# Optimization experiments

Hardware: AMD Instinct MI355X
Metric: run time of the kernel (lower is better)

The kernel has to match this reference:

```python
import jax, jax.numpy as jnp
import numpy as np

FEATURE_SIZES = [300, 1000, 1000, 500, 150, 12, 31, 30, 200, 50000, 50000, 20000, 100000]
# sections per table index i (from feature_sizes_dict -> feature_sections_dict in original)
SECTIONS = [(0, 1), (1, 2), (2, 3), (3, 4), (4, 5), (5, 6), (6, 7), (7, 10),
            (10, 24), (26, 28), (28, 30), (24, 26), (30, 45)]
N, F, E = 8192, 45, 256
_perm, _tbl = [], []
for _i, (_a, _b) in enumerate(SECTIONS):
    for _j in range(_a, _b):
        _perm.append(_j)
        _tbl.append(_i)
PERM = np.array(_perm)              # original Xi column for field position p (concat order)
TBL = np.array(_tbl)                # table index for field position p
OFFSETS = np.concatenate([[0], np.cumsum(FEATURE_SIZES)[:-1]]).astype(np.int32)
FIELD_OFF = OFFSETS[TBL]            # row offset into concatenated table per field position
TOTAL_V = int(np.sum(FEATURE_SIZES))  # 223273
VOCAB_COL = np.zeros(F, np.int32)
VOCAB_COL[PERM] = np.array(FEATURE_SIZES, np.int32)[TBL]  # per-column valid vocab for Xi


def setup_inputs() -> dict:
    key = jax.random.key(0)
    ks = jax.random.split(key, 10)
    Xi = jax.random.randint(ks[0], (N, F), 0, jnp.asarray(VOCAB_COL), dtype=jnp.int32)
    Xv = jax.random.uniform(ks[1], (N, F), dtype=jnp.float32)
    W1 = jax.random.normal(ks[2], (TOTAL_V, 1), dtype=jnp.float32) * 0.01
    W2 = jax.random.normal(ks[3], (TOTAL_V, E), dtype=jnp.float32) * 0.01
    bias = jax.random.normal(ks[4], (1,), dtype=jnp.float32)
    l1_w = jax.random.normal(ks[5], (32, F * E), dtype=jnp.float32) * 0.02
    l1_b = jnp.zeros((32,), jnp.float32)
    l2_w = jax.random.normal(ks[6], (32, 32), dtype=jnp.float32) * 0.02
    l2_b = jnp.zeros((32,), jnp.float32)
    return {"Xi": Xi, "Xv": Xv, "W1": W1, "W2": W2, "bias": bias,
            "l1_w": l1_w, "l1_b": l1_b, "bn1_g": jnp.ones((32,), jnp.float32),
            "bn1_b": jnp.zeros((32,), jnp.float32), "l2_w": l2_w, "l2_b": l2_b,
            "bn2_g": jnp.ones((32,), jnp.float32), "bn2_b": jnp.zeros((32,), jnp.float32)}


def _batchnorm(x, g, b, eps=1e-5):
    # training-mode BN: biased batch statistics (PyTorch normalization convention)
    m = x.mean(0)
    v = x.var(0)
    return (x - m) * jax.lax.rsqrt(v + eps) * g + b


def reference(Xi, Xv, W1, W2, bias, l1_w, l1_b, bn1_g, bn1_b, l2_w, l2_b, bn2_g, bn2_b):
    perm = jnp.asarray(PERM)
    foff = jnp.asarray(FIELD_OFF)
    idx = Xi[:, perm] + foff[None, :]          # (N, 45) rows into concatenated tables
    xv = Xv[:, perm]                            # (N, 45) values in concat order
    # first-order: scalar embedding * value per field
    fm_first = W1[idx, 0] * xv                  # (N, 45)
    # second-order: E-dim embedding * value per field
    e = W2[idx] * xv[:, :, None]                # (N, 45, E)
    s = e.sum(axis=1)                           # (N, E)
    fm_second = 0.5 * (s * s - (e * e).sum(axis=1))  # (N, E)
    # deep part (concat of per-field 2nd-order embs, in original loop order)
    deep = e.reshape(e.shape[0], -1)            # (N, 45*E)
    h = _batchnorm(deep @ l1_w.T + l1_b, bn1_g, bn1_b)
    h = _batchnorm(h @ l2_w.T + l2_b, bn2_g, bn2_b)  # (N, 32); no final num_classes linear in original
    return fm_first.sum(axis=1) + fm_second.sum(axis=1) + h.sum(axis=1) + bias  # (N,)
```

## Files before the change

### kernel.cpp

```cpp
#include <hip/hip_runtime.h>
#include <hip/hip_bf16.h>

#define NS 8192
#define NF 45
#define ED 256
#define L1K 11520
#define NH 32

typedef __attribute__((ext_vector_type(8))) short bf16x8;
typedef __attribute__((ext_vector_type(4))) float f32x4;
typedef __attribute__((ext_vector_type(4))) unsigned uint32x4;

__constant__ int c_perm[NF] = {
    0,1,2,3,4,5,6,7,8,9,
    10,11,12,13,14,15,16,17,18,19,20,21,22,23,
    26,27, 28,29, 24,25,
    30,31,32,33,34,35,36,37,38,39,40,41,42,43,44};
__constant__ int c_foff[NF] = {
    0,300,1300,2300,2800,2950,2962,2993,2993,2993,
    3023,3023,3023,3023,3023,3023,3023,3023,3023,3023,3023,3023,3023,3023,
    3223,3223, 53223,53223, 103223,103223,
    123223,123223,123223,123223,123223,123223,123223,123223,
    123223,123223,123223,123223,123223,123223,123223};

__device__ __forceinline__ short f2bf(float x) {
    unsigned u = __builtin_bit_cast(unsigned, x);
    u += 0x7fffu + ((u >> 16) & 1u);
    return (short)(u >> 16);
}

__device__ __forceinline__ unsigned pk_bf16(float a, float b) {
    unsigned r;
    asm("v_cvt_pk_bf16_f32 %0, %1, %2" : "=v"(r) : "v"(a), "v"(b));
    return r;
}

__global__ __launch_bounds__(256) void k_pack(const float* __restrict__ l1w,
                                              short* __restrict__ bfrag) {
    int t = blockIdx.x * 256 + threadIdx.x;
    if (t >= NF * 8192) return;
    int i  = t & 7;
    int l  = (t >> 3) & 63;
    int nt = (t >> 9) & 1;
    int ks = (t >> 10) & 7;
    int f  = t >> 13;
    int kout = nt * 16 + (l & 15);
    int col  = f * 256 + ks * 32 + (l >> 4) * 8 + i;
    bfrag[t] = f2bf(l1w[kout * L1K + col]);
}

__global__ __launch_bounds__(256, 4) void k_main(const float* __restrict__ W2,
                                                 const float* __restrict__ W1,
                                                 const int* __restrict__ Xi,
                                                 const float* __restrict__ Xv,
                                                 const short* __restrict__ bfrag,
                                                 float* __restrict__ h1h,
                                                 float* __restrict__ parth) {
    __shared__ int   s_idx[16 * NF];
    __shared__ float s_xv [16 * NF];
    __shared__ float s_red[4 * 16 * NH];
    __shared__ float s_q[4][16];
    __shared__ float s_fm1[16];

    const int tid  = threadIdx.x;
    const int w    = tid >> 6;
    const int l    = tid & 63;
    const int m    = l & 15;
    const int g4   = l >> 4;
    const int half = blockIdx.x & 1;
    const int n0   = (blockIdx.x >> 1) * 16;
    const int ks   = half * 4 + w;

    for (int t = tid; t < 16 * NF; t += 256) {
        int f = t % NF;
        int n = n0 + t / NF;
        int col = c_perm[f];
        s_idx[t] = Xi[n * NF + col] + c_foff[f];
        s_xv[t]  = Xv[n * NF + col];
    }
    __syncthreads();

    f32x4 acc0 = {0.f, 0.f, 0.f, 0.f};
    f32x4 acc1 = {0.f, 0.f, 0.f, 0.f};
    float sA[8];
    #pragma unroll
    for (int i = 0; i < 8; ++i) sA[i] = 0.f;
    float esq = 0.f, fm1 = 0.f;

    const short* bbase = bfrag + (size_t)ks * 1024 + l * 8;
    const float* wbase = W2 + ks * 32 + g4 * 8;
    const bool  isw0   = (half == 0 && w == 0);
    const int   mNF    = m * NF;

#define LOADF(ff, A0, A1, B0, B1, XV, W1R)                          \
    do {                                                            \
        int idx_ = s_idx[mNF + (ff)];                               \
        XV = s_xv[mNF + (ff)];                                      \
        const float* wr_ = wbase + (size_t)idx_ * ED;               \
        A0 = *(const f32x4*)(wr_);                                  \
        A1 = *(const f32x4*)(wr_ + 4);                              \
        const short* bp_ = bbase + (size_t)(ff) * 8192;             \
        B0 = *(const bf16x8*)(bp_);                                 \
        B1 = *(const bf16x8*)(bp_ + 512);                           \
        W1R = isw0 ? W1[idx_] : 0.f;                                \
    } while (0)

#define COMPF(A0, A1, B0, B1, XV, W1R)                              \
    do {                                                            \
        float e0 = A0.x * XV, e1 = A0.y * XV, e2 = A0.z * XV, e3 = A0.w * XV; \
        float e4 = A1.x * XV, e5 = A1.y * XV, e6 = A1.z * XV, e7 = A1.w * XV; \
        sA[0] += e0; sA[1] += e1; sA[2] += e2; sA[3] += e3;         \
        sA[4] += e4; sA[5] += e5; sA[6] += e6; sA[7] += e7;         \
        esq += e0 * e0; esq += e1 * e1; esq += e2 * e2; esq += e3 * e3; \
        esq += e4 * e4; esq += e5 * e5; esq += e6 * e6; esq += e7 * e7; \
        uint32x4 au_;                                               \
        au_.x = pk_bf16(e0, e1);                                    \
        au_.y = pk_bf16(e2, e3);                                    \
        au_.z = pk_bf16(e4, e5);                                    \
        au_.w = pk_bf16(e6, e7);                                    \
        bf16x8 Af_ = __builtin_bit_cast(bf16x8, au_);               \
        acc0 = __builtin_amdgcn_mfma_f32_16x16x32_bf16(Af_, B0, acc0, 0, 0, 0); \
        acc1 = __builtin_amdgcn_mfma_f32_16x16x32_bf16(Af_, B1, acc1, 0, 0, 0); \
        fm1 += W1R * XV;                                            \
    } while (0)

    f32x4  A0a, A1a, A0b, A1b, A0c, A1c;
    bf16x8 B0a, B1a, B0b, B1b, B0c, B1c;
    float  XVa, XVb, XVc, W1a, W1b, W1c;

    LOADF(0, A0a, A1a, B0a, B1a, XVa, W1a);
    LOADF(1, A0b, A1b, B0b, B1b, XVb, W1b);
    LOADF(2, A0c, A1c, B0c, B1c, XVc, W1c);

    for (int f = 0; f < NF - 3; f += 3) {
        COMPF(A0a, A1a, B0a, B1a, XVa, W1a);
        LOADF(f + 3, A0a, A1a, B0a, B1a, XVa, W1a);
        COMPF(A0b, A1b, B0b, B1b, XVb, W1b);
        LOADF(f + 4, A0b, A1b, B0b, B1b, XVb, W1b);
        COMPF(A0c, A1c, B0c, B1c, XVc, W1c);
        LOADF(f + 5, A0c, A1c, B0c, B1c, XVc, W1c);
    }
    COMPF(A0a, A1a, B0a, B1a, XVa, W1a);
    COMPF(A0b, A1b, B0b, B1b, XVb, W1b);
    COMPF(A0c, A1c, B0c, B1c, XVc, W1c);

#undef LOADF
#undef COMPF

    float q = -esq;
    #pragma unroll
    for (int i = 0; i < 8; ++i) q += sA[i] * sA[i];
    q += __shfl_xor(q, 16);
    q += __shfl_xor(q, 32);
    if (l < 16) s_q[w][l] = q;
    if (w == 0 && l < 16) s_fm1[l] = fm1;

    #pragma unroll
    for (int r = 0; r < 4; ++r) {
        s_red[w * 512 + (g4 * 4 + r) * 32 +      m] = acc0[r];
        s_red[w * 512 + (g4 * 4 + r) * 32 + 16 + m] = acc1[r];
    }
    __syncthreads();

    float* h1out = h1h + (size_t)half * NS * NH;
    for (int t = tid; t < 512; t += 256) {
        float v = s_red[t] + s_red[512 + t] + s_red[1024 + t] + s_red[1536 + t];
        h1out[(size_t)n0 * NH + t] = v;
    }
    if (tid < 16) {
        float fm2 = 0.5f * (s_q[0][tid] + s_q[1][tid] + s_q[2][tid] + s_q[3][tid]);
        parth[half * NS + n0 + tid] = s_fm1[tid] + fm2;
    }
}

__global__ __launch_bounds__(256) void k_stats(const float* __restrict__ h1h,
                                               float* __restrict__ S1,
                                               float* __restrict__ S2) {
    __shared__ float hc[64 * NH];
    const int tid = threadIdx.x;
    const int base = blockIdx.x * 64;
    for (int t = tid; t < 64 * NH; t += 256)
        hc[t] = h1h[(size_t)base * NH + t] + h1h[(size_t)NS * NH + base * NH + t];
    __syncthreads();

    const int j = tid >> 3;
    const int ks = (tid & 7) * 4;
    float a0 = 0.f, a1 = 0.f, a2 = 0.f, a3 = 0.f;
    for (int n = 0; n < 64; ++n) {
        float hj = hc[n * NH + j];
        f32x4 h = *(const f32x4*)&hc[n * NH + ks];
        a0 += hj * h.x; a1 += hj * h.y; a2 += hj * h.z; a3 += hj * h.w;
    }
    atomicAdd(&S2[j * NH + ks + 0], a0);
    atomicAdd(&S2[j * NH + ks + 1], a1);
    atomicAdd(&S2[j * NH + ks + 2], a2);
    atomicAdd(&S2[j * NH + ks + 3], a3);
    if (tid < NH) {
        float s = 0.f;
        for (int n = 0; n < 64; ++n) s += hc[n * NH + tid];
        atomicAdd(&S1[tid], s);
    }
}

__global__ __launch_bounds__(256) void k_coef(const float* __restrict__ S1,
                                              const float* __restrict__ S2,
                                              const float* __restrict__ g1,
                                              const float* __restrict__ l2w,
                                              const float* __restrict__ g2,
                                              const float* __restrict__ b2,
                                              const float* __restrict__ bias,
                                              float* __restrict__ cvec,
                                              float* __restrict__ k0out) {
    __shared__ float m1[NH], d1[NH], g2r2[NH], csh[NH];
    __shared__ float s2s[NH * NH];
    const int t = threadIdx.x;
    const float invN = 1.f / (float)NS;
    for (int i = t; i < NH * NH; i += 256) s2s[i] = S2[i];
    __syncthreads();
    if (t < NH) {
        float mm = S1[t] * invN;
        float v1 = s2s[t * NH + t] * invN - mm * mm;
        m1[t] = mm;
        d1[t] = g1[t] * rsqrtf(v1 + 1e-5f);
    }
    __syncthreads();
    if (t < NH) {
        float aw[NH];
        float p = 0.f;
        for (int j = 0; j < NH; ++j) { aw[j] = l2w[t * NH + j] * d1[j]; p += aw[j] * m1[j]; }
        float v2 = 0.f;
        for (int j = 0; j < NH; ++j) {
            float acc = 0.f;
            for (int j2 = 0; j2 < NH; ++j2) acc += aw[j2] * s2s[j * NH + j2];
            v2 += aw[j] * acc;
        }
        v2 = v2 * invN - p * p;
        g2r2[t] = g2[t] * rsqrtf(v2 + 1e-5f);
    }
    __syncthreads();
    if (t < NH) {
        float s = 0.f;
        for (int k = 0; k < NH; ++k) s += g2r2[k] * l2w[k * NH + t];
        float c = d1[t] * s;
        csh[t] = c;
        cvec[t] = c;
    }
    __syncthreads();
    if (t == 0) {
        float k0 = bias[0];
        for (int k = 0; k < NH; ++k) k0 += b2[k];
        for (int j = 0; j < NH; ++j) k0 -= csh[j] * m1[j];
        k0out[0] = k0;
    }
}

__global__ __launch_bounds__(256) void k_final(const float* __restrict__ h1h,
                                               const float* __restrict__ parth,
                                               const float* __restrict__ cvec,
                                               const float* __restrict__ k0p,
                                               float* __restrict__ out) {
    __shared__ float c[NH];
    __shared__ float k0s;
    const int t = threadIdx.x;
    if (t < NH) c[t] = cvec[t];
    if (t == 0) k0s = k0p[0];
    __syncthreads();
    const int n = blockIdx.x * 256 + t;
    const f32x4* hp0 = (const f32x4*)(h1h + (size_t)n * NH);
    const f32x4* hp1 = (const f32x4*)(h1h + (size_t)NS * NH + (size_t)n * NH);
    float dot = 0.f;
    #pragma unroll
    for (int q = 0; q < 8; ++q) {
        f32x4 h0 = hp0[q];
        f32x4 h1 = hp1[q];
        dot += (h0.x + h1.x) * c[q * 4]     + (h0.y + h1.y) * c[q * 4 + 1]
             + (h0.z + h1.z) * c[q * 4 + 2] + (h0.w + h1.w) * c[q * 4 + 3];
    }
    out[n] = parth[n] + parth[NS + n] + dot + k0s;
}

extern "C" void kernel_launch(void* const* d_in, const int* in_sizes, int n_in,
                              void* d_out, int out_size, void* d_ws, size_t ws_size,
                              hipStream_t stream) {
    const int*   Xi   = (const int*)  d_in[0];
    const float* Xv   = (const float*)d_in[1];
    const float* W1   = (const float*)d_in[2];
    const float* W2   = (const float*)d_in[3];
    const float* bias = (const float*)d_in[4];
    const float* l1w  = (const float*)d_in[5];
    const float* g1   = (const float*)d_in[7];
    const float* l2w  = (const float*)d_in[9];
    const float* g2   = (const float*)d_in[11];
    const float* b2   = (const float*)d_in[12];
    float* out = (float*)d_out;

    char* ws = (char*)d_ws;
    short* bfrag = (short*)ws;
    float* h1h   = (float*)(ws + (size_t)368640 * 2);
    float* parth = h1h + (size_t)2 * NS * NH;
    float* S1    = parth + 2 * NS;
    float* S2    = S1 + NH;
    float* cvec  = S2 + NH * NH;
    float* k0p   = cvec + NH;

    hipMemsetAsync(S1, 0, (NH + NH * NH) * sizeof(float), stream);
    k_pack <<<(NF * 8192 + 255) / 256, 256, 0, stream>>>(l1w, bfrag);
    k_main <<<NS / 16 * 2, 256, 0, stream>>>(W2, W1, Xi, Xv, bfrag, h1h, parth);
    k_stats<<<128, 256, 0, stream>>>(h1h, S1, S2);
    k_coef <<<1, 256, 0, stream>>>(S1, S2, g1, l2w, g2, b2, bias, cvec, k0p);
    k_final<<<NS / 256, 256, 0, stream>>>(h1h, parth, cvec, k0p, out);
}
```

Before: 380.7 us.

## Process 32 rows per 512-thread block covering full embedding dim, reuse B fragments

Each k_main block now handles 32 samples across all 8 k-slices of the embedding (8 waves) instead of 16 samples split over two half-blocks. Each wave loads a B fragment once and reuses it for two 16-row MFMA groups, halving l1 weight fragment traffic per sample. The result is a single h1h/parth buffer, so the stats and final kernels read half as much. In exchange, register pressure per thread roughly doubles, the grid shrinks to 256 blocks, and the shared reduction across 8 waves is larger.

```diff
diff --git a/kernel.cpp b/kernel.cpp
--- a/kernel.cpp
+++ b/kernel.cpp
@@ -49,29 +49,27 @@
     bfrag[t] = f2bf(l1w[kout * L1K + col]);
 }
 
-__global__ __launch_bounds__(256, 4) void k_main(const float* __restrict__ W2,
+__global__ __launch_bounds__(512, 2) void k_main(const float* __restrict__ W2,
                                                  const float* __restrict__ W1,
                                                  const int* __restrict__ Xi,
                                                  const float* __restrict__ Xv,
                                                  const short* __restrict__ bfrag,
                                                  float* __restrict__ h1h,
                                                  float* __restrict__ parth) {
-    __shared__ int   s_idx[16 * NF];
-    __shared__ float s_xv [16 * NF];
-    __shared__ float s_red[4 * 16 * NH];
-    __shared__ float s_q[4][16];
-    __shared__ float s_fm1[16];
-
-    const int tid  = threadIdx.x;
-    const int w    = tid >> 6;
-    const int l    = tid & 63;
-    const int m    = l & 15;
-    const int g4   = l >> 4;
-    const int half = blockIdx.x & 1;
-    const int n0   = (blockIdx.x >> 1) * 16;
-    const int ks   = half * 4 + w;
-
-    for (int t = tid; t < 16 * NF; t += 256) {
+    __shared__ int   s_idx[32 * NF];
+    __shared__ float s_xv [32 * NF];
+    __shared__ float s_red[8 * 32 * 33];
+    __shared__ float s_q[8 * 32];
+    __shared__ float s_fm1[32];
+
+    const int tid = threadIdx.x;
+    const int w   = tid >> 6;
+    const int l   = tid & 63;
+    const int m   = l & 15;
+    const int g4  = l >> 4;
+    const int n0  = blockIdx.x * 32;
+
+    for (int t = tid; t < 32 * NF; t += 512) {
         int f = t % NF;
         int n = n0 + t / NF;
         int col = c_perm[f];
@@ -80,96 +78,116 @@
     }
     __syncthreads();
 
-    f32x4 acc0 = {0.f, 0.f, 0.f, 0.f};
-    f32x4 acc1 = {0.f, 0.f, 0.f, 0.f};
-    float sA[8];
+    f32x4 acc00 = {0.f,0.f,0.f,0.f}, acc01 = {0.f,0.f,0.f,0.f};
+    f32x4 acc10 = {0.f,0.f,0.f,0.f}, acc11 = {0.f,0.f,0.f,0.f};
+    float sA0[8], sA1[8];
     #pragma unroll
-    for (int i = 0; i < 8; ++i) sA[i] = 0.f;
-    float esq = 0.f, fm1 = 0.f;
-
-    const short* bbase = bfrag + (size_t)ks * 1024 + l * 8;
-    const float* wbase = W2 + ks * 32 + g4 * 8;
-    const bool  isw0   = (half == 0 && w == 0);
+    for (int i = 0; i < 8; ++i) { sA0[i] = 0.f; sA1[i] = 0.f; }
+    float esq0 = 0.f, esq1 = 0.f, fm10 = 0.f, fm11 = 0.f;
+
+    const short* bbase = bfrag + (size_t)w * 1024 + l * 8;
+    const float* wbase = W2 + w * 32 + g4 * 8;
+    const bool  isw0   = (w == 0);
     const int   mNF    = m * NF;
-
-#define LOADF(ff, A0, A1, B0, B1, XV, W1R)                          \
+    const int   mNF1   = (m + 16) * NF;
+
+#define LOADF(ff, A00_,A01_,A10_,A11_,B0_,B1_,XV0_,XV1_,W10_,W11_)  \
     do {                                                            \
-        int idx_ = s_idx[mNF + (ff)];                               \
-        XV = s_xv[mNF + (ff)];                                      \
-        const float* wr_ = wbase + (size_t)idx_ * ED;               \
-        A0 = *(const f32x4*)(wr_);                                  \
-        A1 = *(const f32x4*)(wr_ + 4);                              \
+        int i0_ = s_idx[mNF  + (ff)];                               \
+        int i1_ = s_idx[mNF1 + (ff)];                               \
+        XV0_ = s_xv[mNF  + (ff)];                                   \
+        XV1_ = s_xv[mNF1 + (ff)];                                   \
+        const float* p0_ = wbase + (size_t)i0_ * ED;                \
+        const float* p1_ = wbase + (size_t)i1_ * ED;                \
+        A00_ = *(const f32x4*)(p0_);  A01_ = *(const f32x4*)(p0_ + 4); \
+        A10_ = *(const f32x4*)(p1_);  A11_ = *(const f32x4*)(p1_ + 4); \
         const short* bp_ = bbase + (size_t)(ff) * 8192;             \
-        B0 = *(const bf16x8*)(bp_);                                 \
-        B1 = *(const bf16x8*)(bp_ + 512);                           \
-        W1R = isw0 ? W1[idx_] : 0.f;                                \
+        B0_ = *(const bf16x8*)(bp_);                                \
+        B1_ = *(const bf16x8*)(bp_ + 512);                          \
+        W10_ = isw0 ? W1[i0_] : 0.f;                                \
+        W11_ = isw0 ? W1[i1_] : 0.f;                                \
     } while (0)
 
-#define COMPF(A0, A1, B0, B1, XV, W1R)                              \
+#define COMPG(A0_,A1_,B0_,B1_,XV_,SA_,ESQ_,ACC0_,ACC1_,FM_,W1R_)    \
     do {                                                            \
-        float e0 = A0.x * XV, e1 = A0.y * XV, e2 = A0.z * XV, e3 = A0.w * XV; \
-        float e4 = A1.x * XV, e5 = A1.y * XV, e6 = A1.z * XV, e7 = A1.w * XV; \
-        sA[0] += e0; sA[1] += e1; sA[2] += e2; sA[3] += e3;         \
-        sA[4] += e4; sA[5] += e5; sA[6] += e6; sA[7] += e7;         \
-        esq += e0 * e0; esq += e1 * e1; esq += e2 * e2; esq += e3 * e3; \
-        esq += e4 * e4; esq += e5 * e5; esq += e6 * e6; esq += e7 * e7; \
+        float e0=A0_.x*XV_, e1=A0_.y*XV_, e2=A0_.z*XV_, e3=A0_.w*XV_; \
+        float e4=A1_.x*XV_, e5=A1_.y*XV_, e6=A1_.z*XV_, e7=A1_.w*XV_; \
+        SA_[0]+=e0; SA_[1]+=e1; SA_[2]+=e2; SA_[3]+=e3;             \
+        SA_[4]+=e4; SA_[5]+=e5; SA_[6]+=e6; SA_[7]+=e7;             \
+        ESQ_ += e0*e0; ESQ_ += e1*e1; ESQ_ += e2*e2; ESQ_ += e3*e3; \
+        ESQ_ += e4*e4; ESQ_ += e5*e5; ESQ_ += e6*e6; ESQ_ += e7*e7; \
         uint32x4 au_;                                               \
-        au_.x = pk_bf16(e0, e1);                                    \
-        au_.y = pk_bf16(e2, e3);                                    \
-        au_.z = pk_bf16(e4, e5);                                    \
-        au_.w = pk_bf16(e6, e7);                                    \
+        au_.x = pk_bf16(e0,e1);  au_.y = pk_bf16(e2,e3);            \
+        au_.z = pk_bf16(e4,e5);  au_.w = pk_bf16(e6,e7);            \
         bf16x8 Af_ = __builtin_bit_cast(bf16x8, au_);               \
-        acc0 = __builtin_amdgcn_mfma_f32_16x16x32_bf16(Af_, B0, acc0, 0, 0, 0); \
-        acc1 = __builtin_amdgcn_mfma_f32_16x16x32_bf16(Af_, B1, acc1, 0, 0, 0); \
-        fm1 += W1R * XV;                                            \
+        ACC0_ = __builtin_amdgcn_mfma_f32_16x16x32_bf16(Af_, B0_, ACC0_, 0,0,0); \
+        ACC1_ = __builtin_amdgcn_mfma_f32_16x16x32_bf16(Af_, B1_, ACC1_, 0,0,0); \
+        FM_ += W1R_ * XV_;                                          \
     } while (0)
 
-    f32x4  A0a, A1a, A0b, A1b, A0c, A1c;
-    bf16x8 B0a, B1a, B0b, B1b, B0c, B1c;
-    float  XVa, XVb, XVc, W1a, W1b, W1c;
-
-    LOADF(0, A0a, A1a, B0a, B1a, XVa, W1a);
-    LOADF(1, A0b, A1b, B0b, B1b, XVb, W1b);
-    LOADF(2, A0c, A1c, B0c, B1c, XVc, W1c);
-
-    for (int f = 0; f < NF - 3; f += 3) {
-        COMPF(A0a, A1a, B0a, B1a, XVa, W1a);
-        LOADF(f + 3, A0a, A1a, B0a, B1a, XVa, W1a);
-        COMPF(A0b, A1b, B0b, B1b, XVb, W1b);
-        LOADF(f + 4, A0b, A1b, B0b, B1b, XVb, W1b);
-        COMPF(A0c, A1c, B0c, B1c, XVc, W1c);
-        LOADF(f + 5, A0c, A1c, B0c, B1c, XVc, W1c);
-    }
-    COMPF(A0a, A1a, B0a, B1a, XVa, W1a);
-    COMPF(A0b, A1b, B0b, B1b, XVb, W1b);
-    COMPF(A0c, A1c, B0c, B1c, XVc, W1c);
+#define COMPF(A00_,A01_,A10_,A11_,B0_,B1_,XV0_,XV1_,W10_,W11_)      \
+    do {                                                            \
+        COMPG(A00_,A01_,B0_,B1_,XV0_,sA0,esq0,acc00,acc01,fm10,W10_); \
+        COMPG(A10_,A11_,B0_,B1_,XV1_,sA1,esq1,acc10,acc11,fm11,W11_); \
+    } while (0)
+
+    f32x4  A00a,A01a,A10a,A11a, A00b,A01b,A10b,A11b, A00c,A01c,A10c,A11c;
+    bf16x8 B0a,B1a, B0b,B1b, B0c,B1c;
+    float  XV0a,XV1a, XV0b,XV1b, XV0c,XV1c;
+    float  W10a,W11a, W10b,W11b, W10c,W11c;
+
+    LOADF(0, A00a,A01a,A10a,A11a,B0a,B1a,XV0a,XV1a,W10a,W11a);
+    LOADF(1, A00b,A01b,A10b,A11b,B0b,B1b,XV0b,XV1b,W10b,W11b);
+    LOADF(2, A00c,A01c,A10c,A11c,B0c,B1c,XV0c,XV1c,W10c,W11c);
+
+    for (int f = 0; f + 5 < NF; f += 3) {
+        COMPF(A00a,A01a,A10a,A11a,B0a,B1a,XV0a,XV1a,W10a,W11a);
+        LOADF(f + 3, A00a,A01a,A10a,A11a,B0a,B1a,XV0a,XV1a,W10a,W11a);
+        COMPF(A00b,A01b,A10b,A11b,B0b,B1b,XV0b,XV1b,W10b,W11b);
+        LOADF(f + 4, A00b,A01b,A10b,A11b,B0b,B1b,XV0b,XV1b,W10b,W11b);
+        COMPF(A00c,A01c,A10c,A11c,B0c,B1c,XV0c,XV1c,W10c,W11c);
+        LOADF(f + 5, A00c,A01c,A10c,A11c,B0c,B1c,XV0c,XV1c,W10c,W11c);
+    }
+    COMPF(A00a,A01a,A10a,A11a,B0a,B1a,XV0a,XV1a,W10a,W11a);
+    COMPF(A00b,A01b,A10b,A11b,B0b,B1b,XV0b,XV1b,W10b,W11b);
+    COMPF(A00c,A01c,A10c,A11c,B0c,B1c,XV0c,XV1c,W10c,W11c);
 
 #undef LOADF
+#undef COMPG
 #undef COMPF
 
-    float q = -esq;
+    float q0 = -esq0, q1 = -esq1;
     #pragma unroll
-    for (int i = 0; i < 8; ++i) q += sA[i] * sA[i];
-    q += __shfl_xor(q, 16);
-    q += __shfl_xor(q, 32);
-    if (l < 16) s_q[w][l] = q;
-    if (w == 0 && l < 16) s_fm1[l] = fm1;
+    for (int i = 0; i < 8; ++i) { q0 += sA0[i] * sA0[i]; q1 += sA1[i] * sA1[i]; }
+    q0 += __shfl_xor(q0, 16);  q0 += __shfl_xor(q0, 32);
+    q1 += __shfl_xor(q1, 16);  q1 += __shfl_xor(q1, 32);
+    if (l < 16) {
+        s_q[w * 32 + m]      = q0;
+        s_q[w * 32 + 16 + m] = q1;
+        if (w == 0) { s_fm1[m] = fm10; s_fm1[16 + m] = fm11; }
+    }
 
     #pragma unroll
     for (int r = 0; r < 4; ++r) {
-        s_red[w * 512 + (g4 * 4 + r) * 32 +      m] = acc0[r];
-        s_red[w * 512 + (g4 * 4 + r) * 32 + 16 + m] = acc1[r];
-    }
-    __syncthreads();
-
-    float* h1out = h1h + (size_t)half * NS * NH;
-    for (int t = tid; t < 512; t += 256) {
-        float v = s_red[t] + s_red[512 + t] + s_red[1024 + t] + s_red[1536 + t];
-        h1out[(size_t)n0 * NH + t] = v;
-    }
-    if (tid < 16) {
-        float fm2 = 0.5f * (s_q[0][tid] + s_q[1][tid] + s_q[2][tid] + s_q[3][tid]);
-        parth[half * NS + n0 + tid] = s_fm1[tid] + fm2;
+        s_red[w * 1056 + (g4 * 4 + r) * 33 +      m] = acc00[r];
+        s_red[w * 1056 + (g4 * 4 + r) * 33 + 16 + m] = acc01[r];
+        s_red[w * 1056 + (16 + g4 * 4 + r) * 33 +      m] = acc10[r];
+        s_red[w * 1056 + (16 + g4 * 4 + r) * 33 + 16 + m] = acc11[r];
+    }
+    __syncthreads();
+
+    for (int t = tid; t < 1024; t += 512) {
+        int s = t >> 5, j = t & 31;
+        float v = 0.f;
+        #pragma unroll
+        for (int ww = 0; ww < 8; ++ww) v += s_red[ww * 1056 + s * 33 + j];
+        h1h[(size_t)n0 * NH + t] = v;
+    }
+    if (tid < 32) {
+        float fm2 = 0.f;
+        #pragma unroll
+        for (int ww = 0; ww < 8; ++ww) fm2 += s_q[ww * 32 + tid];
+        parth[n0 + tid] = s_fm1[tid] + 0.5f * fm2;
     }
 }
 
@@ -180,7 +198,7 @@
     const int tid = threadIdx.x;
     const int base = blockIdx.x * 64;
     for (int t = tid; t < 64 * NH; t += 256)
-        hc[t] = h1h[(size_t)base * NH + t] + h1h[(size_t)NS * NH + base * NH + t];
+        hc[t] = h1h[(size_t)base * NH + t];
     __syncthreads();
 
     const int j = tid >> 3;
@@ -267,16 +285,14 @@
     __syncthreads();
     const int n = blockIdx.x * 256 + t;
     const f32x4* hp0 = (const f32x4*)(h1h + (size_t)n * NH);
-    const f32x4* hp1 = (const f32x4*)(h1h + (size_t)NS * NH + (size_t)n * NH);
     float dot = 0.f;
     #pragma unroll
     for (int q = 0; q < 8; ++q) {
         f32x4 h0 = hp0[q];
-        f32x4 h1 = hp1[q];
-        dot += (h0.x + h1.x) * c[q * 4]     + (h0.y + h1.y) * c[q * 4 + 1]
-             + (h0.z + h1.z) * c[q * 4 + 2] + (h0.w + h1.w) * c[q * 4 + 3];
-    }
-    out[n] = parth[n] + parth[NS + n] + dot + k0s;
+        dot += h0.x * c[q * 4]     + h0.y * c[q * 4 + 1]
+             + h0.z * c[q * 4 + 2] + h0.w * c[q * 4 + 3];
+    }
+    out[n] = parth[n] + dot + k0s;
 }
 
 extern "C" void kernel_launch(void* const* d_in, const int* in_sizes, int n_in,
@@ -297,15 +313,15 @@
     char* ws = (char*)d_ws;
     short* bfrag = (short*)ws;
     float* h1h   = (float*)(ws + (size_t)368640 * 2);
-    float* parth = h1h + (size_t)2 * NS * NH;
-    float* S1    = parth + 2 * NS;
+    float* parth = h1h + (size_t)NS * NH;
+    float* S1    = parth + NS;
     float* S2    = S1 + NH;
     float* cvec  = S2 + NH * NH;
     float* k0p   = cvec + NH;
 
     hipMemsetAsync(S1, 0, (NH + NH * NH) * sizeof(float), stream);
     k_pack <<<(NF * 8192 + 255) / 256, 256, 0, stream>>>(l1w, bfrag);
-    k_main <<<NS / 16 * 2, 256, 0, stream>>>(W2, W1, Xi, Xv, bfrag, h1h, parth);
+    k_main <<<NS / 32, 512, 0, stream>>>(W2, W1, Xi, Xv, bfrag, h1h, parth);
     k_stats<<<128, 256, 0, stream>>>(h1h, S1, S2);
     k_coef <<<1, 256, 0, stream>>>(S1, S2, g1, l2w, g2, b2, bias, cvec, k0p);
     k_final<<<NS / 256, 256, 0, stream>>>(h1h, parth, cvec, k0p, out);
```

After: 368.6 us. -3.2%, faster.
